# Optimization experiments

Measured on AMD Instinct MI355X. Metric: run time of the kernel, lower is better.

Reference implementation:

```python
import jax, jax.numpy as jnp
import numpy as np

N_SAMPLES = 8192
EMBED_DIM = 128
NUM_CLASSES = 100


def setup_inputs() -> dict:
    key = jax.random.key(0)
    k1, k2 = jax.random.split(key)
    x = jax.random.normal(k1, (N_SAMPLES, EMBED_DIM), dtype=jnp.float32)
    # FastAP assumes L2-normalized embeddings (dist2 = 2 - 2*cos in [0, 4])
    x = x / jnp.linalg.norm(x, axis=1, keepdims=True)
    labels = jax.random.randint(k2, (N_SAMPLES,), 0, NUM_CLASSES, dtype=jnp.int64 if jax.config.jax_enable_x64 else jnp.int32)
    return {"batch": x, "labels": labels, "num_bins": 10}


def reference(batch, labels, num_bins):
    N = batch.shape[0]
    L = num_bins + 1                      # number of histogram bin centers (edges of linspace)
    Delta = 4.0 / num_bins                # bin width
    Z = jnp.linspace(0.0, 4.0, L)

    same = labels[:, None] == labels[None, :]
    eye = jnp.eye(N, dtype=bool)
    I_pos = (same & ~eye).astype(batch.dtype)   # Aff > 0
    I_neg = (~same).astype(batch.dtype)         # Aff < 0 (diag is 'same', so excluded)
    N_pos = I_pos.sum(axis=1)

    # squared euclidean distance for unit-norm rows: 2 - 2*cos
    dist2 = 2.0 - 2.0 * (batch @ batch.T)       # [N, N]

    # soft-binning histogram: one N x N pulse per bin, reduced to per-row counts.
    # lax.map keeps only one [N, N] pulse buffer alive at a time.
    def bin_fn(z):
        pulse = jnp.maximum(0.0, 1.0 - jnp.abs(dist2 - z) / Delta)
        return (jnp.einsum('ij,ij->i', pulse, I_pos),
                jnp.einsum('ij,ij->i', pulse, I_neg))

    hp, hn = jax.lax.map(bin_fn, Z)             # each [L, N]
    h_pos = hp.T                                # [N, L]
    h_neg = hn.T

    H_pos = jnp.cumsum(h_pos, axis=1)
    H = jnp.cumsum(h_pos + h_neg, axis=1)

    # FastAP = h_pos * H_pos / H, with NaN/Inf (H == 0) zeroed, as in the original
    safe_H = jnp.where(H > 0, H, 1.0)
    ap = jnp.where(H > 0, h_pos * H_pos / safe_H, 0.0).sum(axis=1)

    # divide by N_pos; rows with no positives are dropped from the mean
    valid = N_pos > 0
    safe_Np = jnp.where(valid, N_pos, 1.0)
    ap = jnp.where(valid, ap / safe_Np, 0.0)

    n_valid = valid.sum().astype(batch.dtype)
    loss = 1.0 - ap.sum() / n_valid
    return loss
```

## Files before the change

### kernel.cpp

```cpp
#include <hip/hip_runtime.h>

#define NS 8192
#define EMBED 128
#define ROWCHUNK 512
#define NPANEL (ROWCHUNK / 32)
#define AROW 12
#define INV64K (1.0f / 65536.0f)

typedef __bf16 bf16x8 __attribute__((ext_vector_type(8)));
typedef float f32x4 __attribute__((ext_vector_type(4)));
typedef float f32x2 __attribute__((ext_vector_type(2)));
typedef const __attribute__((address_space(1))) unsigned ag_u32;
typedef __attribute__((address_space(3))) unsigned al_u32;

#define OFF_XB  0u
#define OFF_GS  2097152u
#define OFF_GSP 2228224u
#define OFF_GA  2359296u
#define OFF_GAP 2752512u
#define OFF_CC  3145728u
#define OFF_AC  3146240u
#define ZERO_BYTES 1049120u

__device__ inline unsigned short f2bf(float f) {
  unsigned u = __float_as_uint(f);
  u += 0x7fffu + ((u >> 16) & 1u);
  return (unsigned short)(u >> 16);
}
__device__ inline float clamp01(float x) { return __builtin_amdgcn_fmed3f(x, 0.f, 1.f); }
__device__ inline f32x2 pkclamp01(f32x2 v) {
  return __builtin_elementwise_min(__builtin_elementwise_max(v, (f32x2){0.f, 0.f}),
                                   (f32x2){1.f, 1.f});
}

__global__ __launch_bounds__(256) void prep_kernel(const float* __restrict__ x,
                                                   unsigned short* __restrict__ xb,
                                                   uint4* __restrict__ zbase) {
  const int gid = blockIdx.x * 256 + threadIdx.x;
  const int row = gid >> 4, g = gid & 15;
  const float4 v0 = reinterpret_cast<const float4*>(x)[row * 32 + g * 2];
  const float4 v1 = reinterpret_cast<const float4*>(x)[row * 32 + g * 2 + 1];
  uint4 o;
  o.x = (unsigned)f2bf(v0.x) | ((unsigned)f2bf(v0.y) << 16);
  o.y = (unsigned)f2bf(v0.z) | ((unsigned)f2bf(v0.w) << 16);
  o.z = (unsigned)f2bf(v1.x) | ((unsigned)f2bf(v1.y) << 16);
  o.w = (unsigned)f2bf(v1.z) | ((unsigned)f2bf(v1.w) << 16);
  reinterpret_cast<uint4*>(xb)[row * 16 + (g ^ (row & 7))] = o;
  if (gid < (int)(ZERO_BYTES / 16u)) zbase[gid] = make_uint4(0u, 0u, 0u, 0u);
}

__global__ __launch_bounds__(256, 8) void fastap_main_kernel(
    const unsigned short* __restrict__ xb,
    const int* __restrict__ labels,
    unsigned* __restrict__ gS, unsigned* __restrict__ gSp,
    unsigned* __restrict__ gA, unsigned* __restrict__ gAp,
    int* __restrict__ ccount) {
  __shared__ __align__(16) unsigned short sA[2][32 * 128];
  __shared__ int sLab[ROWCHUNK];

  const int tid  = threadIdx.x;
  const int wave = tid >> 6;
  const int lane = tid & 63;
  const int l16  = lane & 15;
  const int quad = lane >> 4;
  const int colBase  = blockIdx.x * 64;
  const int rowChunk = blockIdx.y * ROWCHUNK;

  if (tid < ROWCHUNK / 4)
    reinterpret_cast<int4*>(sLab)[tid] =
        reinterpret_cast<const int4*>(labels + rowChunk)[tid];

  const int jcol = colBase + wave * 16 + l16;
  bf16x8 bfr[4];
  #pragma unroll
  for (int kb = 0; kb < 4; ++kb) {
    const int pg = (kb * 4 + quad) ^ (l16 & 7);
    bfr[kb] = *reinterpret_cast<const bf16x8*>(&xb[jcol * 128 + pg * 8]);
  }
  const int labj = labels[jcol];

  f32x2 C01 = {0.f, 0.f}, C23 = {0.f, 0.f};
  f32x2 Cp01 = {0.f, 0.f}, Cp23 = {0.f, 0.f};

  int aOff[4];
  #pragma unroll
  for (int kb = 0; kb < 4; ++kb)
    aOff[kb] = l16 * 128 + (((kb * 4 + quad) ^ (l16 & 7)) << 3);

  const unsigned short* xrb = xb + rowChunk * 128;
  auto stage = [&](int p, int b) {
    const unsigned short* src = xrb + p * (32 * 128);
    __builtin_amdgcn_global_load_lds((ag_u32*)(src + tid * 8),
                                     (al_u32*)(&sA[b][tid * 8]), 16, 0, 0);
    __builtin_amdgcn_global_load_lds((ag_u32*)(src + (tid + 256) * 8),
                                     (al_u32*)(&sA[b][(tid + 256) * 8]), 16, 0, 0);
  };

  auto tile16 = [&](const unsigned short* ap, int lcr) {
    const int4 lr = *reinterpret_cast<const int4*>(&sLab[lcr + quad * 4]);
    bf16x8 a0 = *reinterpret_cast<const bf16x8*>(&ap[aOff[0]]);
    bf16x8 a1 = *reinterpret_cast<const bf16x8*>(&ap[aOff[1]]);
    bf16x8 a2 = *reinterpret_cast<const bf16x8*>(&ap[aOff[2]]);
    bf16x8 a3 = *reinterpret_cast<const bf16x8*>(&ap[aOff[3]]);
    f32x4 acc = {0.f, 0.f, 0.f, 0.f};
    acc = __builtin_amdgcn_mfma_f32_16x16x32_bf16(a0, bfr[0], acc, 0, 0, 0);
    acc = __builtin_amdgcn_mfma_f32_16x16x32_bf16(a1, bfr[1], acc, 0, 0, 0);
    acc = __builtin_amdgcn_mfma_f32_16x16x32_bf16(a2, bfr[2], acc, 0, 0, 0);
    acc = __builtin_amdgcn_mfma_f32_16x16x32_bf16(a3, bfr[3], acc, 0, 0, 0);

    const int labr[4] = {lr.x, lr.y, lr.z, lr.w};
    #pragma unroll
    for (int r = 0; r < 4; ++r) {
      const float a = acc[r];
      const float pm = (labr[r] == labj) ? 1.f : 0.f;
      const f32x2 av = {a, a}, p2 = {pm, pm};
      const f32x2 d01 = pkclamp01(__builtin_elementwise_fma(av, (f32x2){5.f, 5.f},
                                                            (f32x2){-1.f, 0.f}));
      const f32x2 d23 = pkclamp01(__builtin_elementwise_fma(av, (f32x2){5.f, 5.f},
                                                            (f32x2){1.f, 2.f}));
      C01 += d01; C23 += d23;
      Cp01 = __builtin_elementwise_fma(p2, d01, Cp01);
      Cp23 = __builtin_elementwise_fma(p2, d23, Cp23);
    }

    const float mabs = fmaxf(fmaxf(fabsf(acc[0]), fabsf(acc[1])),
                             fmaxf(fabsf(acc[2]), fabsf(acc[3])));
    if (__builtin_expect(mabs > 0.4f, 0)) {
      #pragma unroll
      for (int r = 0; r < 4; ++r) {
        const float a = acc[r];
        if (fabsf(a) <= 0.4f) continue;
        const int i = rowChunk + lcr + quad * 4 + r;
        const float d0 = clamp01(fmaf(a, 5.f, -1.f));
        const float d1 = clamp01(a * 5.f);
        const float d2 = clamp01(fmaf(a, 5.f, 1.f));
        const float d3 = clamp01(fmaf(a, 5.f, 2.f));
        if (i == jcol) {
          C01 -= (f32x2){d0, d1};  C23 -= (f32x2){d2, d3};
          Cp01 -= (f32x2){d0, d1}; Cp23 -= (f32x2){d2, d3};
          #pragma unroll
          for (int k = 7; k <= 10; ++k)
            atomicAdd(&gA[jcol * AROW + k], (unsigned)(-65536));
        } else {
          const bool isPos = (labr[r] == labj);
          const float t = fmaf(a, -5.f, 5.f);
          #pragma unroll
          for (int k = 0; k <= 2; ++k) {
            const float v = clamp01((float)(k + 1) - t);
            const int q = (int)(v * 65536.f + 0.5f);
            if (q) {
              atomicAdd(&gA[jcol * AROW + k], (unsigned)q);
              if (isPos) atomicAdd(&gAp[jcol * AROW + k], (unsigned)q);
            }
          }
          #pragma unroll
          for (int k = 7; k <= 10; ++k) {
            const float v = clamp01((float)(k + 1) - t) - 1.f;
            const int q = (int)(v * 65536.f - 0.5f);
            if (q) {
              atomicAdd(&gA[jcol * AROW + k], (unsigned)q);
              if (isPos) atomicAdd(&gAp[jcol * AROW + k], (unsigned)q);
            }
          }
        }
      }
    }
  };

  stage(0, 0);
  __syncthreads();

  if (blockIdx.x == 0) {
    for (int idx = tid; idx < ROWCHUNK; idx += 256)
      atomicAdd(&ccount[sLab[idx]], 1);
  }

  #pragma unroll 1
  for (int p = 0; p < NPANEL; ++p) {
    const int cur = p & 1;
    if (p + 1 < NPANEL) stage(p + 1, cur ^ 1);
    tile16(&sA[cur][0],        p * 32);
    tile16(&sA[cur][16 * 128], p * 32 + 16);
    __syncthreads();
  }

  #pragma unroll
  for (int m = 16; m < 64; m <<= 1) {
    C01.x  += __shfl_xor(C01.x,  m, 64); C01.y  += __shfl_xor(C01.y,  m, 64);
    C23.x  += __shfl_xor(C23.x,  m, 64); C23.y  += __shfl_xor(C23.y,  m, 64);
    Cp01.x += __shfl_xor(Cp01.x, m, 64); Cp01.y += __shfl_xor(Cp01.y, m, 64);
    Cp23.x += __shfl_xor(Cp23.x, m, 64); Cp23.y += __shfl_xor(Cp23.y, m, 64);
  }

  if (quad == 0) {
    const float Cv[4]  = {C01.x, C01.y, C23.x, C23.y};
    const float Cpv[4] = {Cp01.x, Cp01.y, Cp23.x, Cp23.y};
    #pragma unroll
    for (int k = 0; k < 4; ++k) {
      atomicAdd(&gS[jcol * 4 + k],  (unsigned)(int)lrintf(Cv[k]  * 65536.f));
      atomicAdd(&gSp[jcol * 4 + k], (unsigned)(int)lrintf(Cpv[k] * 65536.f));
    }
  }
}

__global__ __launch_bounds__(256) void epilogue_kernel(
    const unsigned* __restrict__ gS, const unsigned* __restrict__ gSp,
    const unsigned* __restrict__ gA, const unsigned* __restrict__ gAp,
    const int* __restrict__ labels, const int* __restrict__ ccount,
    float* __restrict__ accum, unsigned* __restrict__ done,
    float* __restrict__ out) {
  const int i = blockIdx.x * 256 + threadIdx.x;
  const int np = ccount[labels[i]] - 1;
  float ap = 0.f, val = 0.f, HpPrev = 0.f;
  #pragma unroll
  for (int b = 0; b <= 10; ++b) {
    const float baseH  = (b < 3) ? 0.f
                       : (b < 7) ? (float)(int)gS[i * 4 + (b - 3)]  * INV64K : 8192.f;
    const float basePp = (b < 3) ? 0.f
                       : (b < 7) ? (float)(int)gSp[i * 4 + (b - 3)] * INV64K : (float)np;
    const float H  = baseH  + (float)(int)gA[i * AROW + b]  * INV64K;
    const float Hp = basePp + (float)(int)gAp[i * AROW + b] * INV64K;
    const float hp = Hp - HpPrev;
    HpPrev = Hp;
    if (H > 1e-6f) ap += hp * Hp / H;
  }
  if (np > 0) { ap /= (float)np; val = 1.f; } else ap = 0.f;

  __shared__ float sa[256], sv[256];
  sa[threadIdx.x] = ap; sv[threadIdx.x] = val;
  __syncthreads();
  for (int s = 128; s > 0; s >>= 1) {
    if (threadIdx.x < s) {
      sa[threadIdx.x] += sa[threadIdx.x + s];
      sv[threadIdx.x] += sv[threadIdx.x + s];
    }
    __syncthreads();
  }
  if (threadIdx.x == 0) {
    atomicAdd(&accum[0], sa[0]);
    atomicAdd(&accum[1], sv[0]);
    __threadfence();
    const unsigned prev = atomicAdd(done, 1u);
    if (prev == gridDim.x - 1) {
      const float a = atomicAdd(&accum[0], 0.f);
      const float c = atomicAdd(&accum[1], 0.f);
      out[0] = 1.f - (c > 0.f ? a / c : 0.f);
    }
  }
}

extern "C" void kernel_launch(void* const* d_in, const int* in_sizes, int n_in,
                              void* d_out, int out_size, void* d_ws, size_t ws_size,
                              hipStream_t stream) {
  const float* x      = (const float*)d_in[0];
  const int*   labels = (const int*)d_in[1];
  float* out = (float*)d_out;

  char* ws = (char*)d_ws;
  unsigned short* xb = (unsigned short*)(ws + OFF_XB);
  unsigned* gS   = (unsigned*)(ws + OFF_GS);
  unsigned* gSp  = (unsigned*)(ws + OFF_GSP);
  unsigned* gA   = (unsigned*)(ws + OFF_GA);
  unsigned* gAp  = (unsigned*)(ws + OFF_GAP);
  int*      cc   = (int*)(ws + OFF_CC);
  float*    accum = (float*)(ws + OFF_AC);
  unsigned* done  = (unsigned*)(ws + OFF_AC + 8);

  prep_kernel<<<512, 256, 0, stream>>>(x, xb, (uint4*)(ws + OFF_GS));
  fastap_main_kernel<<<dim3(NS / 64, NS / ROWCHUNK), 256, 0, stream>>>(
      xb, labels, gS, gSp, gA, gAp, cc);
  epilogue_kernel<<<NS / 256, 256, 0, stream>>>(gS, gSp, gA, gAp, labels, cc,
                                                accum, done, out);
}
```

Baseline: 113.4 us.

## Load A fragments directly from global into registers, dropping LDS staging

Replaces the double-buffered LDS staging of row panels (global_load_lds plus a per-panel barrier) with direct per-lane global loads of bf16 A fragments into registers, software-pipelined one tile ahead. This removes the LDS traffic and the __syncthreads in the main loop. Each wave now loads its A data independently, so the same rows are fetched four times per block through cache, and register pressure rises. Occupancy in the launch bounds is lowered from 8 to 6 to match.

```diff
diff --git a/kernel.cpp b/kernel.cpp
--- a/kernel.cpp
+++ b/kernel.cpp
@@ -3,15 +3,13 @@
 #define NS 8192
 #define EMBED 128
 #define ROWCHUNK 512
-#define NPANEL (ROWCHUNK / 32)
+#define NTILE (ROWCHUNK / 16)
 #define AROW 12
 #define INV64K (1.0f / 65536.0f)
 
 typedef __bf16 bf16x8 __attribute__((ext_vector_type(8)));
 typedef float f32x4 __attribute__((ext_vector_type(4)));
 typedef float f32x2 __attribute__((ext_vector_type(2)));
-typedef const __attribute__((address_space(1))) unsigned ag_u32;
-typedef __attribute__((address_space(3))) unsigned al_u32;
 
 #define OFF_XB  0u
 #define OFF_GS  2097152u
@@ -49,13 +47,12 @@
   if (gid < (int)(ZERO_BYTES / 16u)) zbase[gid] = make_uint4(0u, 0u, 0u, 0u);
 }
 
-__global__ __launch_bounds__(256, 8) void fastap_main_kernel(
+__global__ __launch_bounds__(256, 6) void fastap_main_kernel(
     const unsigned short* __restrict__ xb,
     const int* __restrict__ labels,
     unsigned* __restrict__ gS, unsigned* __restrict__ gSp,
     unsigned* __restrict__ gA, unsigned* __restrict__ gAp,
     int* __restrict__ ccount) {
-  __shared__ __align__(16) unsigned short sA[2][32 * 128];
   __shared__ int sLab[ROWCHUNK];
 
   const int tid  = threadIdx.x;
@@ -82,31 +79,26 @@
   f32x2 C01 = {0.f, 0.f}, C23 = {0.f, 0.f};
   f32x2 Cp01 = {0.f, 0.f}, Cp23 = {0.f, 0.f};
 
-  int aOff[4];
+  const unsigned short* srcA = xb + (rowChunk + l16) * 128;
+  int go[4];
   #pragma unroll
   for (int kb = 0; kb < 4; ++kb)
-    aOff[kb] = l16 * 128 + (((kb * 4 + quad) ^ (l16 & 7)) << 3);
-
-  const unsigned short* xrb = xb + rowChunk * 128;
-  auto stage = [&](int p, int b) {
-    const unsigned short* src = xrb + p * (32 * 128);
-    __builtin_amdgcn_global_load_lds((ag_u32*)(src + tid * 8),
-                                     (al_u32*)(&sA[b][tid * 8]), 16, 0, 0);
-    __builtin_amdgcn_global_load_lds((ag_u32*)(src + (tid + 256) * 8),
-                                     (al_u32*)(&sA[b][(tid + 256) * 8]), 16, 0, 0);
+    go[kb] = (((kb * 4 + quad) ^ (l16 & 7)) << 3);
+
+  auto loadA = [&](int t, bf16x8* dst) {
+    const unsigned short* p = srcA + t * (16 * 128);
+    #pragma unroll
+    for (int kb = 0; kb < 4; ++kb)
+      dst[kb] = *reinterpret_cast<const bf16x8*>(p + go[kb]);
   };
 
-  auto tile16 = [&](const unsigned short* ap, int lcr) {
+  auto tile16 = [&](const bf16x8* af, int lcr) {
     const int4 lr = *reinterpret_cast<const int4*>(&sLab[lcr + quad * 4]);
-    bf16x8 a0 = *reinterpret_cast<const bf16x8*>(&ap[aOff[0]]);
-    bf16x8 a1 = *reinterpret_cast<const bf16x8*>(&ap[aOff[1]]);
-    bf16x8 a2 = *reinterpret_cast<const bf16x8*>(&ap[aOff[2]]);
-    bf16x8 a3 = *reinterpret_cast<const bf16x8*>(&ap[aOff[3]]);
     f32x4 acc = {0.f, 0.f, 0.f, 0.f};
-    acc = __builtin_amdgcn_mfma_f32_16x16x32_bf16(a0, bfr[0], acc, 0, 0, 0);
-    acc = __builtin_amdgcn_mfma_f32_16x16x32_bf16(a1, bfr[1], acc, 0, 0, 0);
-    acc = __builtin_amdgcn_mfma_f32_16x16x32_bf16(a2, bfr[2], acc, 0, 0, 0);
-    acc = __builtin_amdgcn_mfma_f32_16x16x32_bf16(a3, bfr[3], acc, 0, 0, 0);
+    acc = __builtin_amdgcn_mfma_f32_16x16x32_bf16(af[0], bfr[0], acc, 0, 0, 0);
+    acc = __builtin_amdgcn_mfma_f32_16x16x32_bf16(af[1], bfr[1], acc, 0, 0, 0);
+    acc = __builtin_amdgcn_mfma_f32_16x16x32_bf16(af[2], bfr[2], acc, 0, 0, 0);
+    acc = __builtin_amdgcn_mfma_f32_16x16x32_bf16(af[3], bfr[3], acc, 0, 0, 0);
 
     const int labr[4] = {lr.x, lr.y, lr.z, lr.w};
     #pragma unroll
@@ -167,7 +159,6 @@
     }
   };
 
-  stage(0, 0);
   __syncthreads();
 
   if (blockIdx.x == 0) {
@@ -175,13 +166,14 @@
       atomicAdd(&ccount[sLab[idx]], 1);
   }
 
+  bf16x8 af0[4], af1[4];
+  loadA(0, af0);
   #pragma unroll 1
-  for (int p = 0; p < NPANEL; ++p) {
-    const int cur = p & 1;
-    if (p + 1 < NPANEL) stage(p + 1, cur ^ 1);
-    tile16(&sA[cur][0],        p * 32);
-    tile16(&sA[cur][16 * 128], p * 32 + 16);
-    __syncthreads();
+  for (int t = 0; t < NTILE; t += 2) {
+    loadA(t + 1, af1);
+    tile16(af0, t * 16);
+    loadA((t + 2) & (NTILE - 1), af0);
+    tile16(af1, t * 16 + 16);
   }
 
   #pragma unroll
```

New measurement: 132.1 us. 1.17x slower.

## Compute positive-pair histograms from per-class buckets instead of masking all pairs

Applied to the files above, without the earlier changes.

Prep now groups sample indices into per-class buckets with atomic slot counters. 100 extra blocks each compute all same-class pair dot products with scalar bf16 FMAs and accumulate the positive soft-histogram sums and tail bins. The main MFMA kernel no longer loads labels or does per-element positive masking and accumulation, which cuts its VALU work and register use. The catch is a serial, latency-bound per-class loop, an extra memset, and a hard cap of 256 samples per class that would silently drop samples from larger classes.

```diff
diff --git a/kernel.cpp b/kernel.cpp
--- a/kernel.cpp
+++ b/kernel.cpp
@@ -4,6 +4,8 @@
 #define EMBED 128
 #define ROWCHUNK 512
 #define NPANEL (ROWCHUNK / 32)
+#define NPOSBLK 100
+#define BSTRIDE 256
 #define AROW 12
 #define INV64K (1.0f / 65536.0f)
 
@@ -20,7 +22,8 @@
 #define OFF_GAP 2752512u
 #define OFF_CC  3145728u
 #define OFF_AC  3146240u
-#define ZERO_BYTES 1049120u
+#define OFF_BK  3146752u
+#define ZERO_U4 65536u
 
 __device__ inline unsigned short f2bf(float f) {
   unsigned u = __float_as_uint(f);
@@ -34,8 +37,11 @@
 }
 
 __global__ __launch_bounds__(256) void prep_kernel(const float* __restrict__ x,
+                                                   const int* __restrict__ labels,
                                                    unsigned short* __restrict__ xb,
-                                                   uint4* __restrict__ zbase) {
+                                                   uint4* __restrict__ zbase,
+                                                   int* __restrict__ cnt,
+                                                   int* __restrict__ bucket) {
   const int gid = blockIdx.x * 256 + threadIdx.x;
   const int row = gid >> 4, g = gid & 15;
   const float4 v0 = reinterpret_cast<const float4*>(x)[row * 32 + g * 2];
@@ -46,29 +52,84 @@
   o.z = (unsigned)f2bf(v1.x) | ((unsigned)f2bf(v1.y) << 16);
   o.w = (unsigned)f2bf(v1.z) | ((unsigned)f2bf(v1.w) << 16);
   reinterpret_cast<uint4*>(xb)[row * 16 + (g ^ (row & 7))] = o;
-  if (gid < (int)(ZERO_BYTES / 16u)) zbase[gid] = make_uint4(0u, 0u, 0u, 0u);
+  if (gid < (int)ZERO_U4) zbase[gid] = make_uint4(0u, 0u, 0u, 0u);
+  if (gid < NS) {
+    const int lab = labels[gid];
+    const int slot = atomicAdd(&cnt[lab], 1);
+    if (slot < BSTRIDE) bucket[lab * BSTRIDE + slot] = gid;
+  }
 }
 
 __global__ __launch_bounds__(256, 8) void fastap_main_kernel(
     const unsigned short* __restrict__ xb,
-    const int* __restrict__ labels,
     unsigned* __restrict__ gS, unsigned* __restrict__ gSp,
     unsigned* __restrict__ gA, unsigned* __restrict__ gAp,
-    int* __restrict__ ccount) {
+    const int* __restrict__ cnt, const int* __restrict__ bucket) {
   __shared__ __align__(16) unsigned short sA[2][32 * 128];
-  __shared__ int sLab[ROWCHUNK];
-
-  const int tid  = threadIdx.x;
+
+  const int tid = threadIdx.x;
+
+  if (blockIdx.x < NPOSBLK) {
+    const int c = blockIdx.x;
+    const int n = min(cnt[c], BSTRIDE);
+    const int i = tid;
+    if (i >= n) return;
+    const int gi = bucket[c * BSTRIDE + i];
+    const uint4* pa = reinterpret_cast<const uint4*>(xb + gi * 128);
+    const int sw_a = gi & 7;
+    float B[4] = {0.f, 0.f, 0.f, 0.f};
+    for (int j = 0; j < n; ++j) {
+      if (j == i) continue;
+      const int gj = bucket[c * BSTRIDE + j];
+      const uint4* pb = reinterpret_cast<const uint4*>(xb + gj * 128);
+      const int sw_b = gj & 7;
+      float acc = 0.f;
+      #pragma unroll
+      for (int g = 0; g < 16; ++g) {
+        const uint4 av = pa[g ^ sw_a];
+        const uint4 bv = pb[g ^ sw_b];
+        const unsigned au[4] = {av.x, av.y, av.z, av.w};
+        const unsigned bu[4] = {bv.x, bv.y, bv.z, bv.w};
+        #pragma unroll
+        for (int w = 0; w < 4; ++w) {
+          acc = fmaf(__uint_as_float(au[w] << 16),
+                     __uint_as_float(bu[w] << 16), acc);
+          acc = fmaf(__uint_as_float(au[w] & 0xffff0000u),
+                     __uint_as_float(bu[w] & 0xffff0000u), acc);
+        }
+      }
+      const float a = acc;
+      B[0] += clamp01(fmaf(a, 5.f, -1.f));
+      B[1] += clamp01(a * 5.f);
+      B[2] += clamp01(fmaf(a, 5.f, 1.f));
+      B[3] += clamp01(fmaf(a, 5.f, 2.f));
+      if (__builtin_expect(fabsf(a) > 0.4f, 0)) {
+        const float t = fmaf(a, -5.f, 5.f);
+        #pragma unroll
+        for (int k = 0; k <= 2; ++k) {
+          const int q = (int)(clamp01((float)(k + 1) - t) * 65536.f + 0.5f);
+          if (q) atomicAdd(&gAp[gi * AROW + k], (unsigned)q);
+        }
+        #pragma unroll
+        for (int k = 7; k <= 10; ++k) {
+          const int q = (int)((clamp01((float)(k + 1) - t) - 1.f) * 65536.f - 0.5f);
+          if (q) atomicAdd(&gAp[gi * AROW + k], (unsigned)q);
+        }
+      }
+    }
+    #pragma unroll
+    for (int k = 0; k < 4; ++k)
+      atomicAdd(&gSp[gi * 4 + k], (unsigned)(int)lrintf(B[k] * 65536.f));
+    return;
+  }
+
+  const int mb   = blockIdx.x - NPOSBLK;
   const int wave = tid >> 6;
   const int lane = tid & 63;
   const int l16  = lane & 15;
   const int quad = lane >> 4;
-  const int colBase  = blockIdx.x * 64;
-  const int rowChunk = blockIdx.y * ROWCHUNK;
-
-  if (tid < ROWCHUNK / 4)
-    reinterpret_cast<int4*>(sLab)[tid] =
-        reinterpret_cast<const int4*>(labels + rowChunk)[tid];
+  const int colBase  = (mb & 127) * 64;
+  const int rowChunk = (mb >> 7) * ROWCHUNK;
 
   const int jcol = colBase + wave * 16 + l16;
   bf16x8 bfr[4];
@@ -77,10 +138,8 @@
     const int pg = (kb * 4 + quad) ^ (l16 & 7);
     bfr[kb] = *reinterpret_cast<const bf16x8*>(&xb[jcol * 128 + pg * 8]);
   }
-  const int labj = labels[jcol];
 
   f32x2 C01 = {0.f, 0.f}, C23 = {0.f, 0.f};
-  f32x2 Cp01 = {0.f, 0.f}, Cp23 = {0.f, 0.f};
 
   int aOff[4];
   #pragma unroll
@@ -97,7 +156,6 @@
   };
 
   auto tile16 = [&](const unsigned short* ap, int lcr) {
-    const int4 lr = *reinterpret_cast<const int4*>(&sLab[lcr + quad * 4]);
     bf16x8 a0 = *reinterpret_cast<const bf16x8*>(&ap[aOff[0]]);
     bf16x8 a1 = *reinterpret_cast<const bf16x8*>(&ap[aOff[1]]);
     bf16x8 a2 = *reinterpret_cast<const bf16x8*>(&ap[aOff[2]]);
@@ -108,19 +166,13 @@
     acc = __builtin_amdgcn_mfma_f32_16x16x32_bf16(a2, bfr[2], acc, 0, 0, 0);
     acc = __builtin_amdgcn_mfma_f32_16x16x32_bf16(a3, bfr[3], acc, 0, 0, 0);
 
-    const int labr[4] = {lr.x, lr.y, lr.z, lr.w};
     #pragma unroll
     for (int r = 0; r < 4; ++r) {
-      const float a = acc[r];
-      const float pm = (labr[r] == labj) ? 1.f : 0.f;
-      const f32x2 av = {a, a}, p2 = {pm, pm};
-      const f32x2 d01 = pkclamp01(__builtin_elementwise_fma(av, (f32x2){5.f, 5.f},
-                                                            (f32x2){-1.f, 0.f}));
-      const f32x2 d23 = pkclamp01(__builtin_elementwise_fma(av, (f32x2){5.f, 5.f},
-                                                            (f32x2){1.f, 2.f}));
-      C01 += d01; C23 += d23;
-      Cp01 = __builtin_elementwise_fma(p2, d01, Cp01);
-      Cp23 = __builtin_elementwise_fma(p2, d23, Cp23);
+      const f32x2 av = {acc[r], acc[r]};
+      C01 += pkclamp01(__builtin_elementwise_fma(av, (f32x2){5.f, 5.f},
+                                                 (f32x2){-1.f, 0.f}));
+      C23 += pkclamp01(__builtin_elementwise_fma(av, (f32x2){5.f, 5.f},
+                                                 (f32x2){1.f, 2.f}));
     }
 
     const float mabs = fmaxf(fmaxf(fabsf(acc[0]), fabsf(acc[1])),
@@ -137,30 +189,20 @@
         const float d3 = clamp01(fmaf(a, 5.f, 2.f));
         if (i == jcol) {
           C01 -= (f32x2){d0, d1};  C23 -= (f32x2){d2, d3};
-          Cp01 -= (f32x2){d0, d1}; Cp23 -= (f32x2){d2, d3};
           #pragma unroll
           for (int k = 7; k <= 10; ++k)
             atomicAdd(&gA[jcol * AROW + k], (unsigned)(-65536));
         } else {
-          const bool isPos = (labr[r] == labj);
           const float t = fmaf(a, -5.f, 5.f);
           #pragma unroll
           for (int k = 0; k <= 2; ++k) {
-            const float v = clamp01((float)(k + 1) - t);
-            const int q = (int)(v * 65536.f + 0.5f);
-            if (q) {
-              atomicAdd(&gA[jcol * AROW + k], (unsigned)q);
-              if (isPos) atomicAdd(&gAp[jcol * AROW + k], (unsigned)q);
-            }
+            const int q = (int)(clamp01((float)(k + 1) - t) * 65536.f + 0.5f);
+            if (q) atomicAdd(&gA[jcol * AROW + k], (unsigned)q);
           }
           #pragma unroll
           for (int k = 7; k <= 10; ++k) {
-            const float v = clamp01((float)(k + 1) - t) - 1.f;
-            const int q = (int)(v * 65536.f - 0.5f);
-            if (q) {
-              atomicAdd(&gA[jcol * AROW + k], (unsigned)q);
-              if (isPos) atomicAdd(&gAp[jcol * AROW + k], (unsigned)q);
-            }
+            const int q = (int)((clamp01((float)(k + 1) - t) - 1.f) * 65536.f - 0.5f);
+            if (q) atomicAdd(&gA[jcol * AROW + k], (unsigned)q);
           }
         }
       }
@@ -169,11 +211,6 @@
 
   stage(0, 0);
   __syncthreads();
-
-  if (blockIdx.x == 0) {
-    for (int idx = tid; idx < ROWCHUNK; idx += 256)
-      atomicAdd(&ccount[sLab[idx]], 1);
-  }
 
   #pragma unroll 1
   for (int p = 0; p < NPANEL; ++p) {
@@ -186,31 +223,26 @@
 
   #pragma unroll
   for (int m = 16; m < 64; m <<= 1) {
-    C01.x  += __shfl_xor(C01.x,  m, 64); C01.y  += __shfl_xor(C01.y,  m, 64);
-    C23.x  += __shfl_xor(C23.x,  m, 64); C23.y  += __shfl_xor(C23.y,  m, 64);
-    Cp01.x += __shfl_xor(Cp01.x, m, 64); Cp01.y += __shfl_xor(Cp01.y, m, 64);
-    Cp23.x += __shfl_xor(Cp23.x, m, 64); Cp23.y += __shfl_xor(Cp23.y, m, 64);
+    C01.x += __shfl_xor(C01.x, m, 64); C01.y += __shfl_xor(C01.y, m, 64);
+    C23.x += __shfl_xor(C23.x, m, 64); C23.y += __shfl_xor(C23.y, m, 64);
   }
 
   if (quad == 0) {
-    const float Cv[4]  = {C01.x, C01.y, C23.x, C23.y};
-    const float Cpv[4] = {Cp01.x, Cp01.y, Cp23.x, Cp23.y};
+    const float Cv[4] = {C01.x, C01.y, C23.x, C23.y};
     #pragma unroll
-    for (int k = 0; k < 4; ++k) {
-      atomicAdd(&gS[jcol * 4 + k],  (unsigned)(int)lrintf(Cv[k]  * 65536.f));
-      atomicAdd(&gSp[jcol * 4 + k], (unsigned)(int)lrintf(Cpv[k] * 65536.f));
-    }
+    for (int k = 0; k < 4; ++k)
+      atomicAdd(&gS[jcol * 4 + k], (unsigned)(int)lrintf(Cv[k] * 65536.f));
   }
 }
 
 __global__ __launch_bounds__(256) void epilogue_kernel(
     const unsigned* __restrict__ gS, const unsigned* __restrict__ gSp,
     const unsigned* __restrict__ gA, const unsigned* __restrict__ gAp,
-    const int* __restrict__ labels, const int* __restrict__ ccount,
+    const int* __restrict__ labels, const int* __restrict__ cnt,
     float* __restrict__ accum, unsigned* __restrict__ done,
     float* __restrict__ out) {
   const int i = blockIdx.x * 256 + threadIdx.x;
-  const int np = ccount[labels[i]] - 1;
+  const int np = cnt[labels[i]] - 1;
   float ap = 0.f, val = 0.f, HpPrev = 0.f;
   #pragma unroll
   for (int b = 0; b <= 10; ++b) {
@@ -262,13 +294,16 @@
   unsigned* gSp  = (unsigned*)(ws + OFF_GSP);
   unsigned* gA   = (unsigned*)(ws + OFF_GA);
   unsigned* gAp  = (unsigned*)(ws + OFF_GAP);
-  int*      cc   = (int*)(ws + OFF_CC);
+  int*      cnt  = (int*)(ws + OFF_CC);
   float*    accum = (float*)(ws + OFF_AC);
   unsigned* done  = (unsigned*)(ws + OFF_AC + 8);
-
-  prep_kernel<<<512, 256, 0, stream>>>(x, xb, (uint4*)(ws + OFF_GS));
-  fastap_main_kernel<<<dim3(NS / 64, NS / ROWCHUNK), 256, 0, stream>>>(
-      xb, labels, gS, gSp, gA, gAp, cc);
-  epilogue_kernel<<<NS / 256, 256, 0, stream>>>(gS, gSp, gA, gAp, labels, cc,
+  int*      bucket = (int*)(ws + OFF_BK);
+
+  hipMemsetAsync(ws + OFF_CC, 0, 1024, stream);
+  prep_kernel<<<512, 256, 0, stream>>>(x, labels, xb, (uint4*)(ws + OFF_GS),
+                                       cnt, bucket);
+  fastap_main_kernel<<<NPOSBLK + (NS / 64) * (NS / ROWCHUNK), 256, 0, stream>>>(
+      xb, gS, gSp, gA, gAp, cnt, bucket);
+  epilogue_kernel<<<NS / 256, 256, 0, stream>>>(gS, gSp, gA, gAp, labels, cnt,
                                                 accum, done, out);
 }
```

Result: slower. 289.7 us (+155.5%).

## Sort samples by class so tiles skip positive-mask work outside class range

Applied to the files above, without the earlier changes.

Adds a counting pass that groups rows by label, then scatters the bf16 embeddings into class-sorted order and records each row's class. In the main kernel, positives become a contiguous index range [lo,hi), so most 16-row tiles take a cheaper path that only accumulates the total histogram and skips the per-element label compare and positive FMAs. Label loads into LDS and the per-block class count atomics are removed. The cost is a single-block serial counting kernel with a serial prefix scan, plus one extra launch, which sits on the critical path ahead of the main kernel.

```diff
diff --git a/kernel.cpp b/kernel.cpp
--- a/kernel.cpp
+++ b/kernel.cpp
@@ -13,31 +13,55 @@
 typedef const __attribute__((address_space(1))) unsigned ag_u32;
 typedef __attribute__((address_space(3))) unsigned al_u32;
 
-#define OFF_XB  0u
-#define OFF_GS  2097152u
-#define OFF_GSP 2228224u
-#define OFF_GA  2359296u
-#define OFF_GAP 2752512u
-#define OFF_CC  3145728u
-#define OFF_AC  3146240u
-#define ZERO_BYTES 1049120u
-
+#define OFF_XB    0u
+#define OFF_GS    2097152u
+#define OFF_GSP   2228224u
+#define OFF_GA    2359296u
+#define OFF_GAP   2752512u
+#define OFF_AC    3145728u
+#define OFF_CNT   3145792u
+#define OFF_OFS   3146304u
+#define OFF_INTRA 3146816u
+#define OFF_CLS   3179584u
+#define ZERO_U4   65537u
+
+__device__ inline float clamp01(float x) { return __builtin_amdgcn_fmed3f(x, 0.f, 1.f); }
+__device__ inline f32x2 pkclamp01(f32x2 v) {
+  return __builtin_elementwise_min(__builtin_elementwise_max(v, (f32x2){0.f, 0.f}),
+                                   (f32x2){1.f, 1.f});
+}
 __device__ inline unsigned short f2bf(float f) {
   unsigned u = __float_as_uint(f);
   u += 0x7fffu + ((u >> 16) & 1u);
   return (unsigned short)(u >> 16);
 }
-__device__ inline float clamp01(float x) { return __builtin_amdgcn_fmed3f(x, 0.f, 1.f); }
-__device__ inline f32x2 pkclamp01(f32x2 v) {
-  return __builtin_elementwise_min(__builtin_elementwise_max(v, (f32x2){0.f, 0.f}),
-                                   (f32x2){1.f, 1.f});
-}
-
-__global__ __launch_bounds__(256) void prep_kernel(const float* __restrict__ x,
-                                                   unsigned short* __restrict__ xb,
-                                                   uint4* __restrict__ zbase) {
+
+__global__ __launch_bounds__(256) void prep_count_kernel(const int* __restrict__ labels,
+                                                         int* __restrict__ cnt,
+                                                         int* __restrict__ ofs,
+                                                         int* __restrict__ intra) {
+  __shared__ int c[128];
+  const int tid = threadIdx.x;
+  if (tid < 128) c[tid] = 0;
+  __syncthreads();
+  for (int i = tid; i < NS; i += 256)
+    intra[i] = atomicAdd(&c[labels[i]], 1);
+  __syncthreads();
+  if (tid == 0) {
+    int run = 0;
+    for (int k = 0; k < 128; ++k) { ofs[k] = run; cnt[k] = c[k]; run += c[k]; }
+  }
+}
+
+__global__ __launch_bounds__(256) void prep_scatter_kernel(
+    const float* __restrict__ x, const int* __restrict__ labels,
+    const int* __restrict__ ofs, const int* __restrict__ intra,
+    unsigned short* __restrict__ xb, int* __restrict__ classOf,
+    uint4* __restrict__ zbase) {
   const int gid = blockIdx.x * 256 + threadIdx.x;
   const int row = gid >> 4, g = gid & 15;
+  const int lab = labels[row];
+  const int slot = ofs[lab] + intra[row];
   const float4 v0 = reinterpret_cast<const float4*>(x)[row * 32 + g * 2];
   const float4 v1 = reinterpret_cast<const float4*>(x)[row * 32 + g * 2 + 1];
   uint4 o;
@@ -45,18 +69,18 @@
   o.y = (unsigned)f2bf(v0.z) | ((unsigned)f2bf(v0.w) << 16);
   o.z = (unsigned)f2bf(v1.x) | ((unsigned)f2bf(v1.y) << 16);
   o.w = (unsigned)f2bf(v1.z) | ((unsigned)f2bf(v1.w) << 16);
-  reinterpret_cast<uint4*>(xb)[row * 16 + (g ^ (row & 7))] = o;
-  if (gid < (int)(ZERO_BYTES / 16u)) zbase[gid] = make_uint4(0u, 0u, 0u, 0u);
+  reinterpret_cast<uint4*>(xb)[slot * 16 + (g ^ (slot & 7))] = o;
+  if (g == 0) classOf[slot] = lab;
+  if (gid < (int)ZERO_U4) zbase[gid] = make_uint4(0u, 0u, 0u, 0u);
 }
 
 __global__ __launch_bounds__(256, 8) void fastap_main_kernel(
     const unsigned short* __restrict__ xb,
-    const int* __restrict__ labels,
+    const int* __restrict__ classOf, const int* __restrict__ cnt,
+    const int* __restrict__ ofs,
     unsigned* __restrict__ gS, unsigned* __restrict__ gSp,
-    unsigned* __restrict__ gA, unsigned* __restrict__ gAp,
-    int* __restrict__ ccount) {
+    unsigned* __restrict__ gA, unsigned* __restrict__ gAp) {
   __shared__ __align__(16) unsigned short sA[2][32 * 128];
-  __shared__ int sLab[ROWCHUNK];
 
   const int tid  = threadIdx.x;
   const int wave = tid >> 6;
@@ -66,10 +90,6 @@
   const int colBase  = blockIdx.x * 64;
   const int rowChunk = blockIdx.y * ROWCHUNK;
 
-  if (tid < ROWCHUNK / 4)
-    reinterpret_cast<int4*>(sLab)[tid] =
-        reinterpret_cast<const int4*>(labels + rowChunk)[tid];
-
   const int jcol = colBase + wave * 16 + l16;
   bf16x8 bfr[4];
   #pragma unroll
@@ -77,7 +97,9 @@
     const int pg = (kb * 4 + quad) ^ (l16 & 7);
     bfr[kb] = *reinterpret_cast<const bf16x8*>(&xb[jcol * 128 + pg * 8]);
   }
-  const int labj = labels[jcol];
+  const int ci = classOf[jcol];
+  const int lo = ofs[ci];
+  const int hi = lo + cnt[ci];
 
   f32x2 C01 = {0.f, 0.f}, C23 = {0.f, 0.f};
   f32x2 Cp01 = {0.f, 0.f}, Cp23 = {0.f, 0.f};
@@ -97,7 +119,6 @@
   };
 
   auto tile16 = [&](const unsigned short* ap, int lcr) {
-    const int4 lr = *reinterpret_cast<const int4*>(&sLab[lcr + quad * 4]);
     bf16x8 a0 = *reinterpret_cast<const bf16x8*>(&ap[aOff[0]]);
     bf16x8 a1 = *reinterpret_cast<const bf16x8*>(&ap[aOff[1]]);
     bf16x8 a2 = *reinterpret_cast<const bf16x8*>(&ap[aOff[2]]);
@@ -108,19 +129,32 @@
     acc = __builtin_amdgcn_mfma_f32_16x16x32_bf16(a2, bfr[2], acc, 0, 0, 0);
     acc = __builtin_amdgcn_mfma_f32_16x16x32_bf16(a3, bfr[3], acc, 0, 0, 0);
 
-    const int labr[4] = {lr.x, lr.y, lr.z, lr.w};
-    #pragma unroll
-    for (int r = 0; r < 4; ++r) {
-      const float a = acc[r];
-      const float pm = (labr[r] == labj) ? 1.f : 0.f;
-      const f32x2 av = {a, a}, p2 = {pm, pm};
-      const f32x2 d01 = pkclamp01(__builtin_elementwise_fma(av, (f32x2){5.f, 5.f},
-                                                            (f32x2){-1.f, 0.f}));
-      const f32x2 d23 = pkclamp01(__builtin_elementwise_fma(av, (f32x2){5.f, 5.f},
-                                                            (f32x2){1.f, 2.f}));
-      C01 += d01; C23 += d23;
-      Cp01 = __builtin_elementwise_fma(p2, d01, Cp01);
-      Cp23 = __builtin_elementwise_fma(p2, d23, Cp23);
+    const int i0 = rowChunk + lcr + quad * 4;
+
+    if (__builtin_expect((hi > i0) & (lo < i0 + 4), 0)) {
+      #pragma unroll
+      for (int r = 0; r < 4; ++r) {
+        const float a = acc[r];
+        const int i = i0 + r;
+        const float pm = (i >= lo && i < hi) ? 1.f : 0.f;
+        const f32x2 av = {a, a}, p2 = {pm, pm};
+        const f32x2 d01 = pkclamp01(__builtin_elementwise_fma(av, (f32x2){5.f, 5.f},
+                                                              (f32x2){-1.f, 0.f}));
+        const f32x2 d23 = pkclamp01(__builtin_elementwise_fma(av, (f32x2){5.f, 5.f},
+                                                              (f32x2){1.f, 2.f}));
+        C01 += d01; C23 += d23;
+        Cp01 = __builtin_elementwise_fma(p2, d01, Cp01);
+        Cp23 = __builtin_elementwise_fma(p2, d23, Cp23);
+      }
+    } else {
+      #pragma unroll
+      for (int r = 0; r < 4; ++r) {
+        const f32x2 av = {acc[r], acc[r]};
+        C01 += pkclamp01(__builtin_elementwise_fma(av, (f32x2){5.f, 5.f},
+                                                   (f32x2){-1.f, 0.f}));
+        C23 += pkclamp01(__builtin_elementwise_fma(av, (f32x2){5.f, 5.f},
+                                                   (f32x2){1.f, 2.f}));
+      }
     }
 
     const float mabs = fmaxf(fmaxf(fabsf(acc[0]), fabsf(acc[1])),
@@ -130,7 +164,7 @@
       for (int r = 0; r < 4; ++r) {
         const float a = acc[r];
         if (fabsf(a) <= 0.4f) continue;
-        const int i = rowChunk + lcr + quad * 4 + r;
+        const int i = i0 + r;
         const float d0 = clamp01(fmaf(a, 5.f, -1.f));
         const float d1 = clamp01(a * 5.f);
         const float d2 = clamp01(fmaf(a, 5.f, 1.f));
@@ -142,12 +176,11 @@
           for (int k = 7; k <= 10; ++k)
             atomicAdd(&gA[jcol * AROW + k], (unsigned)(-65536));
         } else {
-          const bool isPos = (labr[r] == labj);
+          const bool isPos = (i >= lo) & (i < hi);
           const float t = fmaf(a, -5.f, 5.f);
           #pragma unroll
           for (int k = 0; k <= 2; ++k) {
-            const float v = clamp01((float)(k + 1) - t);
-            const int q = (int)(v * 65536.f + 0.5f);
+            const int q = (int)(clamp01((float)(k + 1) - t) * 65536.f + 0.5f);
             if (q) {
               atomicAdd(&gA[jcol * AROW + k], (unsigned)q);
               if (isPos) atomicAdd(&gAp[jcol * AROW + k], (unsigned)q);
@@ -155,8 +188,7 @@
           }
           #pragma unroll
           for (int k = 7; k <= 10; ++k) {
-            const float v = clamp01((float)(k + 1) - t) - 1.f;
-            const int q = (int)(v * 65536.f - 0.5f);
+            const int q = (int)((clamp01((float)(k + 1) - t) - 1.f) * 65536.f - 0.5f);
             if (q) {
               atomicAdd(&gA[jcol * AROW + k], (unsigned)q);
               if (isPos) atomicAdd(&gAp[jcol * AROW + k], (unsigned)q);
@@ -170,11 +202,6 @@
   stage(0, 0);
   __syncthreads();
 
-  if (blockIdx.x == 0) {
-    for (int idx = tid; idx < ROWCHUNK; idx += 256)
-      atomicAdd(&ccount[sLab[idx]], 1);
-  }
-
   #pragma unroll 1
   for (int p = 0; p < NPANEL; ++p) {
     const int cur = p & 1;
@@ -206,11 +233,11 @@
 __global__ __launch_bounds__(256) void epilogue_kernel(
     const unsigned* __restrict__ gS, const unsigned* __restrict__ gSp,
     const unsigned* __restrict__ gA, const unsigned* __restrict__ gAp,
-    const int* __restrict__ labels, const int* __restrict__ ccount,
+    const int* __restrict__ classOf, const int* __restrict__ cnt,
     float* __restrict__ accum, unsigned* __restrict__ done,
     float* __restrict__ out) {
   const int i = blockIdx.x * 256 + threadIdx.x;
-  const int np = ccount[labels[i]] - 1;
+  const int np = cnt[classOf[i]] - 1;
   float ap = 0.f, val = 0.f, HpPrev = 0.f;
   #pragma unroll
   for (int b = 0; b <= 10; ++b) {
@@ -258,17 +285,22 @@
 
   char* ws = (char*)d_ws;
   unsigned short* xb = (unsigned short*)(ws + OFF_XB);
-  unsigned* gS   = (unsigned*)(ws + OFF_GS);
-  unsigned* gSp  = (unsigned*)(ws + OFF_GSP);
-  unsigned* gA   = (unsigned*)(ws + OFF_GA);
-  unsigned* gAp  = (unsigned*)(ws + OFF_GAP);
-  int*      cc   = (int*)(ws + OFF_CC);
+  unsigned* gS    = (unsigned*)(ws + OFF_GS);
+  unsigned* gSp   = (unsigned*)(ws + OFF_GSP);
+  unsigned* gA    = (unsigned*)(ws + OFF_GA);
+  unsigned* gAp   = (unsigned*)(ws + OFF_GAP);
   float*    accum = (float*)(ws + OFF_AC);
   unsigned* done  = (unsigned*)(ws + OFF_AC + 8);
-
-  prep_kernel<<<512, 256, 0, stream>>>(x, xb, (uint4*)(ws + OFF_GS));
+  int*      cnt   = (int*)(ws + OFF_CNT);
+  int*      ofs   = (int*)(ws + OFF_OFS);
+  int*      intra = (int*)(ws + OFF_INTRA);
+  int*      cls   = (int*)(ws + OFF_CLS);
+
+  prep_count_kernel<<<1, 256, 0, stream>>>(labels, cnt, ofs, intra);
+  prep_scatter_kernel<<<512, 256, 0, stream>>>(x, labels, ofs, intra, xb, cls,
+                                               (uint4*)(ws + OFF_GS));
   fastap_main_kernel<<<dim3(NS / 64, NS / ROWCHUNK), 256, 0, stream>>>(
-      xb, labels, gS, gSp, gA, gAp, cc);
-  epilogue_kernel<<<NS / 256, 256, 0, stream>>>(gS, gSp, gA, gAp, labels, cc,
+      xb, cls, cnt, ofs, gS, gSp, gA, gAp);
+  epilogue_kernel<<<NS / 256, 256, 0, stream>>>(gS, gSp, gA, gAp, cls, cnt,
                                                 accum, done, out);
 }
```

Result: slower. 118.2 us (+4.2%).
